# Performance work log

Hardware: AMD Instinct MI355X
Metric: run time of the kernel (lower is better)

Reference implementation:

```python
import jax, jax.numpy as jnp
import numpy as np

N = 100_000      # nodes
E = 1_600_000    # directed input edges (no self loops, unique canonical pairs)
F_IN = 256       # num_features
HID = 128        # 2 * num_hidden (GATConv out width)
NHID = 64        # num_hidden
C = 4            # num_classes
G = 128          # number of graphs in the batch
NEG_SLOPE = 0.2  # PyG GATConv default LeakyReLU slope


def setup_inputs() -> dict:
    key = jax.random.key(0)
    ks = jax.random.split(key, 16)

    # --- graph structure (numpy; deduped canonical pairs so that
    # concat(e, reversed(e)) exactly matches PyG to_undirected+coalesce) ---
    rng = np.random.RandomState(0)
    n_cand = int(E * 1.05)
    s = rng.randint(0, N, size=n_cand)
    off = rng.randint(1, N, size=n_cand)
    d = (s + off) % N                      # guarantees no self loops
    lo, hi = np.minimum(s, d), np.maximum(s, d)
    pairs = np.unique(lo.astype(np.int64) * N + hi.astype(np.int64))[:E]
    src = (pairs // N).astype(np.int64)
    dst = (pairs % N).astype(np.int64)
    edge_index = jnp.asarray(np.stack([src, dst]))  # [2, E]

    batch = jnp.sort(jax.random.randint(ks[0], (N,), 0, G)).astype(jnp.int64)
    x = jax.random.normal(ks[1], (N, F_IN), dtype=jnp.float32)

    sc = 0.05
    params = dict(
        W1=jax.random.normal(ks[2], (HID, F_IN)) * sc,
        as1=jax.random.normal(ks[3], (HID,)) * sc,
        ad1=jax.random.normal(ks[4], (HID,)) * sc,
        b1=jnp.zeros((HID,), jnp.float32),
        W2=jax.random.normal(ks[5], (HID, HID)) * sc,
        as2=jax.random.normal(ks[6], (HID,)) * sc,
        ad2=jax.random.normal(ks[7], (HID,)) * sc,
        b2=jnp.zeros((HID,), jnp.float32),
        fw1=jax.random.normal(ks[8], (NHID, HID)) * sc,
        fb1=jnp.zeros((NHID,), jnp.float32),
        fw2=jax.random.normal(ks[9], (C, NHID)) * sc,
        fb2=jnp.zeros((C,), jnp.float32),
    )
    return dict(x=x, edge_index=edge_index, batch=batch, **params)


def _gat_conv(h_in, src, dst, W, a_src, a_dst, bias):
    """PyG GATConv, heads=1, concat=True. src/dst include self loops."""
    h = h_in @ W.T                                        # [N, out]
    # per-edge attention logits: a_src . h_j + a_dst . h_i
    e = jax.nn.leaky_relu((h @ a_src)[src] + (h @ a_dst)[dst], NEG_SLOPE)
    # edge softmax over incoming edges of each dst node
    m = jax.ops.segment_max(e, dst, num_segments=N)       # [N]
    w = jnp.exp(e - m[dst])
    denom = jax.ops.segment_sum(w, dst, num_segments=N)   # [N] (>0: self loops)
    alpha = w / denom[dst]                                # [Etot]
    out = jax.ops.segment_sum(h[src] * alpha[:, None], dst, num_segments=N)
    return out + bias


def reference(x, edge_index, batch,
              W1, as1, ad1, b1, W2, as2, ad2, b2,
              fw1, fb1, fw2, fb2):
    # to_undirected: input has unique canonical (lo<hi) pairs -> concat exact
    s0, d0 = edge_index[0], edge_index[1]
    loop = jnp.arange(N, dtype=s0.dtype)
    src = jnp.concatenate([s0, d0, loop])  # GATConv adds self loops
    dst = jnp.concatenate([d0, s0, loop])

    h = jax.nn.selu(_gat_conv(x, src, dst, W1, as1, ad1, b1))
    h = jax.nn.selu(_gat_conv(h, src, dst, W2, as2, ad2, b2))

    # global mean pool over graphs
    sums = jax.ops.segment_sum(h, batch, num_segments=G)            # [G, HID]
    cnt = jax.ops.segment_sum(jnp.ones((N,), h.dtype), batch, num_segments=G)
    g = jax.nn.selu(sums / jnp.maximum(cnt, 1.0)[:, None])

    g = jax.nn.selu(g @ fw1.T + fb1)
    # dropout p=0.5 is identity in eval mode
    logits = g @ fw2.T + fb2
    return jax.nn.log_softmax(logits, axis=-1)                      # [G, C]
```

## Files before the change

### kernel.cpp

```cpp
#include <hip/hip_runtime.h>
#include <hip/hip_bf16.h>


#define NN 100000
#define EE 1600000
#define GG 128
#define HID 128
#define AGG_CAP 512
#define NEG_SLOPE 0.2f

typedef short bf16x8 __attribute__((ext_vector_type(8)));
typedef float f32x4 __attribute__((ext_vector_type(4)));

__device__ __forceinline__ float lrelu(float x) { return x > 0.f ? x : NEG_SLOPE * x; }

__device__ __forceinline__ float selu(float x) {
    const float sc = 1.0507009873554805f, al = 1.6732632423543772f;
    return x > 0.f ? sc * x : sc * al * (__expf(x) - 1.f);
}

__device__ __forceinline__ unsigned short f2bf(float x) {
    unsigned int b = __float_as_uint(x);
    b += 0x7FFFu + ((b >> 16) & 1u);
    return (unsigned short)(b >> 16);
}


__global__ __launch_bounds__(256) void castbf_kernel(const float* __restrict__ in,
                                                     unsigned short* __restrict__ out, int n) {
    int i = (blockIdx.x * blockDim.x + threadIdx.x) * 4;
    if (i >= n) return;
    float4 v = *reinterpret_cast<const float4*>(in + i);
    union { unsigned short u[4]; uint2 w; } pk;
    pk.u[0] = f2bf(v.x); pk.u[1] = f2bf(v.y); pk.u[2] = f2bf(v.z); pk.u[3] = f2bf(v.w);
    *reinterpret_cast<uint2*>(out + i) = pk.w;
}


__global__ __launch_bounds__(256) void loptr_kernel(const int* __restrict__ ei,
                                                    int* __restrict__ loptr, int n, int E_) {
    int v = blockIdx.x * blockDim.x + threadIdx.x;
    if (v > n) return;
    int lo = 0, hi = E_;
    while (lo < hi) {
        int mid = (lo + hi) >> 1;
        if (ei[mid] < v) lo = mid + 1; else hi = mid;
    }
    loptr[v] = lo;
}


__global__ void count_kernel(const int* __restrict__ ei, int* __restrict__ deg, int E_) {
    int e = blockIdx.x * blockDim.x + threadIdx.x;
    if (e >= E_) return;
    atomicAdd(&deg[ei[E_ + e]], 1);
}

#define SCAN_CHUNK 512

__global__ __launch_bounds__(256) void block_sum_kernel(const int* __restrict__ deg,
                                                        int* __restrict__ bsum, int n) {
    __shared__ int sd[256];
    int b = blockIdx.x, t = threadIdx.x;
    int base = b * SCAN_CHUNK;
    int v = 0;
    int i0 = base + t, i1 = base + t + 256;
    if (i0 < n) v += deg[i0];
    if (i1 < n) v += deg[i1];
    sd[t] = v;
    __syncthreads();
    for (int off = 128; off; off >>= 1) {
        if (t < off) sd[t] += sd[t + off];
        __syncthreads();
    }
    if (t == 0) bsum[b] = sd[0];
}

__global__ __launch_bounds__(256) void top_scan_kernel(const int* __restrict__ bsum,
                                                       int* __restrict__ boff, int nb,
                                                       int* __restrict__ total_out) {
    __shared__ int a[256], b[256];
    int t = threadIdx.x;
    int v = (t < nb) ? bsum[t] : 0;
    int* cur = a; int* nxt = b;
    cur[t] = v;
    __syncthreads();
    for (int off = 1; off < 256; off <<= 1) {
        int val = cur[t] + ((t >= off) ? cur[t - off] : 0);
        nxt[t] = val;
        __syncthreads();
        int* tmp = cur; cur = nxt; nxt = tmp;
    }
    if (t < nb) boff[t] = cur[t] - v;
    if (t == nb - 1) *total_out = cur[t];
}

__global__ __launch_bounds__(512) void scan_final_kernel(const int* __restrict__ deg,
                                                         const int* __restrict__ boff,
                                                         int* __restrict__ row_ptr,
                                                         int* __restrict__ cursor, int n) {
    __shared__ int a[512], b[512];
    int blk = blockIdx.x, t = threadIdx.x;
    int i = blk * 512 + t;
    int v = (i < n) ? deg[i] : 0;
    int orig = v;
    int* cur = a; int* nxt = b;
    cur[t] = v;
    __syncthreads();
    for (int off = 1; off < 512; off <<= 1) {
        int val = cur[t] + ((t >= off) ? cur[t - off] : 0);
        nxt[t] = val;
        __syncthreads();
        int* tmp = cur; cur = nxt; nxt = tmp;
    }
    if (i < n) {
        int excl = cur[t] - orig + boff[blk];
        row_ptr[i] = excl;
        cursor[i] = excl;
    }
}

__global__ void scatter_kernel(const int* __restrict__ ei, int* __restrict__ cursor,
                               int* __restrict__ csr, int E_) {
    int e = blockIdx.x * blockDim.x + threadIdx.x;
    if (e >= E_) return;
    int u = ei[e], v = ei[E_ + e];
    int p = atomicAdd(&cursor[v], 1);
    csr[p] = u;
}


template<int K, bool BF16IN>
__global__ __launch_bounds__(256) void mfma_gemm(const void* __restrict__ Ain,
                                                 const unsigned short* __restrict__ Wb,
                                                 float* __restrict__ C,
                                                 unsigned short* __restrict__ Cb,
                                                 int M) {
    __shared__ unsigned short As[128 * 32];
    __shared__ unsigned short Bs[128 * 32];
    int tid = threadIdx.x;
    int brow = blockIdx.x * 128;
    int w = tid >> 6, lane = tid & 63;
    int wr = (w >> 1) * 64, wc = (w & 1) * 64;
    int l15 = lane & 15, g = lane >> 4;

    const f32x4 zero = {0.f, 0.f, 0.f, 0.f};
    f32x4 acc[4][4];
    #pragma unroll
    for (int m = 0; m < 4; ++m)
        #pragma unroll
        for (int n = 0; n < 4; ++n) acc[m][n] = zero;

    int srow = tid >> 2;
    int slot = tid & 3;

    for (int k0 = 0; k0 < K; k0 += 32) {
        #pragma unroll
        for (int half = 0; half < 2; ++half) {
            int r = srow + half * 64;
            int grow = brow + r;
            union { unsigned short u[8]; uint4 v; } pk;
            if (BF16IN) {
                const unsigned short* A16 = (const unsigned short*)Ain;
                if (grow < M)
                    pk.v = *reinterpret_cast<const uint4*>(A16 + (size_t)grow * K + k0 + slot * 8);
                else pk.v = make_uint4(0, 0, 0, 0);
            } else {
                const float* A32 = (const float*)Ain;
                if (grow < M) {
                    const float4* p = reinterpret_cast<const float4*>(A32 + (size_t)grow * K + k0 + slot * 8);
                    float4 f0 = p[0], f1 = p[1];
                    pk.u[0] = f2bf(f0.x); pk.u[1] = f2bf(f0.y);
                    pk.u[2] = f2bf(f0.z); pk.u[3] = f2bf(f0.w);
                    pk.u[4] = f2bf(f1.x); pk.u[5] = f2bf(f1.y);
                    pk.u[6] = f2bf(f1.z); pk.u[7] = f2bf(f1.w);
                } else pk.v = make_uint4(0, 0, 0, 0);
            }
            int ss = slot ^ (r & 3);
            *reinterpret_cast<uint4*>(&As[r * 32 + ss * 8]) = pk.v;
        }
        #pragma unroll
        for (int half = 0; half < 2; ++half) {
            int r = srow + half * 64;
            uint4 v = *reinterpret_cast<const uint4*>(Wb + (size_t)r * K + k0 + slot * 8);
            int ss = slot ^ (r & 3);
            *reinterpret_cast<uint4*>(&Bs[r * 32 + ss * 8]) = v;
        }
        __syncthreads();

        bf16x8 af[4], bfr[4];
        #pragma unroll
        for (int m = 0; m < 4; ++m) {
            int row = wr + m * 16 + l15;
            af[m] = *reinterpret_cast<const bf16x8*>(&As[row * 32 + ((g ^ (row & 3)) * 8)]);
        }
        #pragma unroll
        for (int n = 0; n < 4; ++n) {
            int col = wc + n * 16 + l15;
            bfr[n] = *reinterpret_cast<const bf16x8*>(&Bs[col * 32 + ((g ^ (col & 3)) * 8)]);
        }
        #pragma unroll
        for (int m = 0; m < 4; ++m)
            #pragma unroll
            for (int n = 0; n < 4; ++n)
                acc[m][n] = __builtin_amdgcn_mfma_f32_16x16x32_bf16(af[m], bfr[n], acc[m][n], 0, 0, 0);
        __syncthreads();
    }

    #pragma unroll
    for (int m = 0; m < 4; ++m) {
        int rbase = brow + wr + m * 16 + g * 4;
        #pragma unroll
        for (int j = 0; j < 4; ++j) {
            int row = rbase + j;
            if (row < M) {
                #pragma unroll
                for (int n = 0; n < 4; ++n) {
                    int col = wc + n * 16 + l15;
                    float val = acc[m][n][j];
                    C[(size_t)row * 128 + col] = val;
                    Cb[(size_t)row * 128 + col] = f2bf(val);
                }
            }
        }
    }
}


__global__ __launch_bounds__(256) void hshd_kernel(const float* __restrict__ h,
                                                   const float* __restrict__ a_src,
                                                   const float* __restrict__ a_dst,
                                                   float* __restrict__ hs, float* __restrict__ hd,
                                                   int n) {
    int w = (blockIdx.x * blockDim.x + threadIdx.x) >> 6;
    int lane = threadIdx.x & 63;
    if (w >= n) return;
    float2 hv = reinterpret_cast<const float2*>(h + (size_t)w * 128)[lane];
    float2 as2 = reinterpret_cast<const float2*>(a_src)[lane];
    float2 ad2 = reinterpret_cast<const float2*>(a_dst)[lane];
    float ps = hv.x * as2.x + hv.y * as2.y;
    float pd = hv.x * ad2.x + hv.y * ad2.y;
    #pragma unroll
    for (int off = 32; off; off >>= 1) {
        ps += __shfl_xor(ps, off);
        pd += __shfl_xor(pd, off);
    }
    if (lane == 0) { hs[w] = ps; hd[w] = pd; }
}


__global__ __launch_bounds__(256) void agg_kernel(const float* __restrict__ h,
                                                  const unsigned int* __restrict__ hb32,
                                                  const float* __restrict__ hs,
                                                  const float* __restrict__ hd,
                                                  const int* __restrict__ loptr,
                                                  const int* __restrict__ eiD,
                                                  const int* __restrict__ hiptr,
                                                  const int* __restrict__ csr,
                                                  const float* __restrict__ bias,
                                                  float* __restrict__ out,
                                                  unsigned int* __restrict__ outb,
                                                  int n) {
    __shared__ float esh[4][AGG_CAP];
    __shared__ int ush[4][AGG_CAP];
    int wib = threadIdx.x >> 6;
    int lane = threadIdx.x & 63;
    int v = blockIdx.x * 4 + wib;
    if (v >= n) return;
    int s_lo = loptr[v];
    int dlo = loptr[v + 1] - s_lo;
    int s_hi = hiptr[v];
    int d = dlo + (hiptr[v + 1] - s_hi);
    float hdv = hd[v];
    float e_self = lrelu(hs[v] + hdv);
    float m, inv;
    bool fits = (d <= AGG_CAP);

    auto nbr = [&](int k) -> int {
        return (k < dlo) ? eiD[s_lo + k] : csr[s_hi + k - dlo];
    };
    auto gx = [&](int u) -> float2 {
        unsigned int w = hb32[(size_t)u * 64 + lane];
        return make_float2(__uint_as_float(w << 16), __uint_as_float(w & 0xFFFF0000u));
    };

    if (fits) {
        float mloc = -3.4e38f;
        for (int k = lane; k < d; k += 64) {
            int u = nbr(k);
            float e = lrelu(hs[u] + hdv);
            ush[wib][k] = u;
            esh[wib][k] = e;
            mloc = fmaxf(mloc, e);
        }
        #pragma unroll
        for (int off = 32; off; off >>= 1) mloc = fmaxf(mloc, __shfl_xor(mloc, off));
        m = fmaxf(mloc, e_self);
        float sloc = 0.f;
        for (int k = lane; k < d; k += 64) sloc += __expf(esh[wib][k] - m);
        #pragma unroll
        for (int off = 32; off; off >>= 1) sloc += __shfl_xor(sloc, off);
        float s = sloc + __expf(e_self - m);
        inv = 1.f / s;
        for (int k = lane; k < d; k += 64) esh[wib][k] = __expf(esh[wib][k] - m) * inv;
    } else {
        float mloc = -3.4e38f;
        for (int k = lane; k < d; k += 64) mloc = fmaxf(mloc, lrelu(hs[nbr(k)] + hdv));
        #pragma unroll
        for (int off = 32; off; off >>= 1) mloc = fmaxf(mloc, __shfl_xor(mloc, off));
        m = fmaxf(mloc, e_self);
        float sloc = 0.f;
        for (int k = lane; k < d; k += 64) sloc += __expf(lrelu(hs[nbr(k)] + hdv) - m);
        #pragma unroll
        for (int off = 32; off; off >>= 1) sloc += __shfl_xor(sloc, off);
        float s = sloc + __expf(e_self - m);
        inv = 1.f / s;
    }
    __syncthreads();

    float2 hvv = reinterpret_cast<const float2*>(h + (size_t)v * 128)[lane];
    float a_self = __expf(e_self - m) * inv;
    float accx = a_self * hvv.x;
    float accy = a_self * hvv.y;
    if (fits) {
        int k = 0;
        for (; k + 4 <= d; k += 4) {
            float a0 = esh[wib][k + 0], a1 = esh[wib][k + 1];
            float a2 = esh[wib][k + 2], a3 = esh[wib][k + 3];
            int u0 = ush[wib][k + 0], u1 = ush[wib][k + 1];
            int u2 = ush[wib][k + 2], u3 = ush[wib][k + 3];
            float2 x0 = gx(u0);
            float2 x1 = gx(u1);
            float2 x2 = gx(u2);
            float2 x3 = gx(u3);
            accx = fmaf(a0, x0.x, accx); accy = fmaf(a0, x0.y, accy);
            accx = fmaf(a1, x1.x, accx); accy = fmaf(a1, x1.y, accy);
            accx = fmaf(a2, x2.x, accx); accy = fmaf(a2, x2.y, accy);
            accx = fmaf(a3, x3.x, accx); accy = fmaf(a3, x3.y, accy);
        }
        for (; k < d; ++k) {
            float al = esh[wib][k];
            float2 xv = gx(ush[wib][k]);
            accx = fmaf(al, xv.x, accx);
            accy = fmaf(al, xv.y, accy);
        }
    } else {
        for (int k = 0; k < d; ++k) {
            int u = nbr(k);
            float al = __expf(lrelu(hs[u] + hdv) - m) * inv;
            float2 xv = gx(u);
            accx = fmaf(al, xv.x, accx);
            accy = fmaf(al, xv.y, accy);
        }
    }
    float2 bb = reinterpret_cast<const float2*>(bias)[lane];
    float o0 = selu(accx + bb.x);
    float o1 = selu(accy + bb.y);
    reinterpret_cast<float2*>(out + (size_t)v * 128)[lane] = make_float2(o0, o1);
    unsigned int pb = ((unsigned int)f2bf(o1) << 16) | (unsigned int)f2bf(o0);
    outb[(size_t)v * 64 + lane] = pb;
}


__device__ __forceinline__ int lower_bound_dev(const int* __restrict__ b, int n, int val) {
    int lo = 0, hi = n;
    while (lo < hi) {
        int mid = (lo + hi) >> 1;
        if (b[mid] < val) lo = mid + 1; else hi = mid;
    }
    return lo;
}

__global__ __launch_bounds__(1024) void pool_mlp_kernel(const float* __restrict__ h,
                                                        const int* __restrict__ batch,
                                                        const float* __restrict__ fw1,
                                                        const float* __restrict__ fb1,
                                                        const float* __restrict__ fw2,
                                                        const float* __restrict__ fb2,
                                                        float* __restrict__ out, int n) {
    int g = blockIdx.x;
    int t = threadIdx.x;
    int lane = t & 63;
    int rg = t >> 6;
    __shared__ float2 sm[16][64];
    __shared__ float gv[128];
    __shared__ float hid[64];
    __shared__ float logits[4];

    int s = lower_bound_dev(batch, n, g);
    int e = lower_bound_dev(batch, n, g + 1);

    float2 acc = make_float2(0.f, 0.f);
    const float2* h2 = reinterpret_cast<const float2*>(h);
    int i = s + rg;
    for (; i + 16 < e; i += 32) {
        float2 v0 = h2[(size_t)i * 64 + lane];
        float2 v1 = h2[(size_t)(i + 16) * 64 + lane];
        acc.x += v0.x + v1.x;
        acc.y += v0.y + v1.y;
    }
    for (; i < e; i += 16) {
        float2 v0 = h2[(size_t)i * 64 + lane];
        acc.x += v0.x;
        acc.y += v0.y;
    }
    sm[rg][lane] = acc;
    __syncthreads();
    if (rg == 0) {
        float2 tot = make_float2(0.f, 0.f);
        #pragma unroll
        for (int r = 0; r < 16; ++r) {
            tot.x += sm[r][lane].x;
            tot.y += sm[r][lane].y;
        }
        float cnt = fmaxf((float)(e - s), 1.0f);
        gv[lane * 2 + 0] = selu(tot.x / cnt);
        gv[lane * 2 + 1] = selu(tot.y / cnt);
    }
    __syncthreads();
    if (t < 64) {
        float a = fb1[t];
        for (int k = 0; k < 128; ++k) a = fmaf(fw1[t * 128 + k], gv[k], a);
        hid[t] = selu(a);
    }
    __syncthreads();
    if (t < 4) {
        float a = fb2[t];
        for (int k = 0; k < 64; ++k) a = fmaf(fw2[t * 64 + k], hid[k], a);
        logits[t] = a;
    }
    __syncthreads();
    if (t < 4) {
        float mx = fmaxf(fmaxf(logits[0], logits[1]), fmaxf(logits[2], logits[3]));
        float sum = __expf(logits[0] - mx) + __expf(logits[1] - mx) +
                    __expf(logits[2] - mx) + __expf(logits[3] - mx);
        out[g * 4 + t] = logits[t] - mx - logf(sum);
    }
}


extern "C" void kernel_launch(void* const* d_in, const int* in_sizes, int n_in,
                              void* d_out, int out_size, void* d_ws, size_t ws_size,
                              hipStream_t stream) {
    const float* x   = (const float*)d_in[0];
    const int*   ei  = (const int*)d_in[1];
    const int*   bat = (const int*)d_in[2];
    const float* W1  = (const float*)d_in[3];
    const float* as1 = (const float*)d_in[4];
    const float* ad1 = (const float*)d_in[5];
    const float* b1  = (const float*)d_in[6];
    const float* W2  = (const float*)d_in[7];
    const float* as2 = (const float*)d_in[8];
    const float* ad2 = (const float*)d_in[9];
    const float* b2  = (const float*)d_in[10];
    const float* fw1 = (const float*)d_in[11];
    const float* fb1 = (const float*)d_in[12];
    const float* fw2 = (const float*)d_in[13];
    const float* fb2 = (const float*)d_in[14];
    float* out = (float*)d_out;

    char* ws = (char*)d_ws;
    size_t off = 0;
    auto alloc = [&](size_t bytes) {
        void* p = ws + off;
        off += (bytes + 255) & ~(size_t)255;
        return p;
    };
    float*          bufA    = (float*)alloc((size_t)NN * 128 * 4);
    float*          bufB    = (float*)alloc((size_t)NN * 128 * 4);
    unsigned short* hb      = (unsigned short*)alloc((size_t)NN * 128 * 2);
    unsigned short* hbB     = (unsigned short*)alloc((size_t)NN * 128 * 2);
    unsigned short* wb1     = (unsigned short*)alloc((size_t)HID * 256 * 2);
    unsigned short* wb2     = (unsigned short*)alloc((size_t)HID * 128 * 2);
    float*          hs      = (float*)alloc((size_t)NN * 4);
    float*          hd      = (float*)alloc((size_t)NN * 4);
    int*            deg     = (int*)alloc((size_t)NN * 4);
    int*            row_ptr = (int*)alloc((size_t)(NN + 1) * 4);
    int*            cursor  = (int*)alloc((size_t)NN * 4);
    int*            loptr   = (int*)alloc((size_t)(NN + 1) * 4);
    int*            csr     = (int*)alloc((size_t)EE * 4);
    int*            bsum    = (int*)alloc(256 * 4);
    int*            boff    = (int*)alloc(256 * 4);

    hipMemsetAsync(deg, 0, (size_t)NN * 4, stream);
    loptr_kernel<<<(NN + 1 + 255) / 256, 256, 0, stream>>>(ei, loptr, NN, EE);
    count_kernel<<<(EE + 255) / 256, 256, 0, stream>>>(ei, deg, EE);
    int NB = (NN + SCAN_CHUNK - 1) / SCAN_CHUNK;
    block_sum_kernel<<<NB, 256, 0, stream>>>(deg, bsum, NN);
    top_scan_kernel<<<1, 256, 0, stream>>>(bsum, boff, NB, row_ptr + NN);
    scan_final_kernel<<<NB, 512, 0, stream>>>(deg, boff, row_ptr, cursor, NN);
    scatter_kernel<<<(EE + 255) / 256, 256, 0, stream>>>(ei, cursor, csr, EE);

    castbf_kernel<<<(HID * 256 / 4 + 255) / 256, 256, 0, stream>>>(W1, wb1, HID * 256);
    castbf_kernel<<<(HID * 128 / 4 + 255) / 256, 256, 0, stream>>>(W2, wb2, HID * 128);

    const int* eiD = ei + EE;
    int gemmGrid = (NN + 127) / 128;

    mfma_gemm<256, false><<<gemmGrid, 256, 0, stream>>>(x, wb1, bufA, hb, NN);
    hshd_kernel<<<((size_t)NN * 64 + 255) / 256, 256, 0, stream>>>(bufA, as1, ad1, hs, hd, NN);
    agg_kernel<<<(NN + 3) / 4, 256, 0, stream>>>(bufA, (const unsigned int*)hb, hs, hd,
                                                 loptr, eiD, row_ptr, csr, b1, bufB,
                                                 (unsigned int*)hbB, NN);

    mfma_gemm<128, true><<<gemmGrid, 256, 0, stream>>>(hbB, wb2, bufA, hb, NN);
    hshd_kernel<<<((size_t)NN * 64 + 255) / 256, 256, 0, stream>>>(bufA, as2, ad2, hs, hd, NN);
    agg_kernel<<<(NN + 3) / 4, 256, 0, stream>>>(bufA, (const unsigned int*)hb, hs, hd,
                                                 loptr, eiD, row_ptr, csr, b2, bufB,
                                                 (unsigned int*)hbB, NN);

    pool_mlp_kernel<<<GG, 1024, 0, stream>>>(bufB, bat, fw1, fb1, fw2, fb2, out, NN);
}
```

Before: 739.8 us.

## Two-pass bucketed CSR scatter and deepen aggregation gather unroll

The single random scatter that builds the CSR is replaced by two passes. Edges are first binned into 128-node destination buckets via per-bucket atomic cursors into a temporary (u,v) array, then a second pass does the per-node atomic placement. Because bucketed edges are locally clustered, the second pass's atomics and csr writes should hit nearby addresses. The aggregation inner loop is also unrolled from 4 to 8 neighbors to put more gathers in flight, at the cost of an extra 12.8MB temp buffer, two extra launches and higher register pressure.

```diff
diff --git a/kernel.cpp b/kernel.cpp
--- a/kernel.cpp
+++ b/kernel.cpp
@@ -8,6 +8,8 @@
 #define HID 128
 #define AGG_CAP 512
 #define NEG_SLOPE 0.2f
+#define BKT_SHIFT 7
+#define NBKT ((NN + 127) >> 7)
 
 typedef short bf16x8 __attribute__((ext_vector_type(8)));
 typedef float f32x4 __attribute__((ext_vector_type(4)));
@@ -120,13 +122,32 @@
     }
 }
 
-__global__ void scatter_kernel(const int* __restrict__ ei, int* __restrict__ cursor,
-                               int* __restrict__ csr, int E_) {
+
+__global__ __launch_bounds__(256) void bcur_init_kernel(const int* __restrict__ row_ptr,
+                                                        int* __restrict__ bcur) {
+    int b = blockIdx.x * blockDim.x + threadIdx.x;
+    if (b < NBKT) bcur[b] = row_ptr[b << BKT_SHIFT];
+}
+
+__global__ __launch_bounds__(256) void binA_kernel(const int* __restrict__ ei,
+                                                   int* __restrict__ bcur,
+                                                   uint2* __restrict__ tmp, int E_) {
     int e = blockIdx.x * blockDim.x + threadIdx.x;
     if (e >= E_) return;
     int u = ei[e], v = ei[E_ + e];
-    int p = atomicAdd(&cursor[v], 1);
-    csr[p] = u;
+    int b = v >> BKT_SHIFT;
+    int p = atomicAdd(&bcur[b], 1);
+    tmp[p] = make_uint2((unsigned)u, (unsigned)v);
+}
+
+__global__ __launch_bounds__(256) void binB_kernel(const uint2* __restrict__ tmp,
+                                                   int* __restrict__ cursor,
+                                                   int* __restrict__ csr, int E_) {
+    int i = blockIdx.x * blockDim.x + threadIdx.x;
+    if (i >= E_) return;
+    uint2 t = tmp[i];
+    int p = atomicAdd(&cursor[t.y], 1);
+    csr[p] = (int)t.x;
 }
 
 
@@ -324,19 +345,17 @@
     float accy = a_self * hvv.y;
     if (fits) {
         int k = 0;
-        for (; k + 4 <= d; k += 4) {
-            float a0 = esh[wib][k + 0], a1 = esh[wib][k + 1];
-            float a2 = esh[wib][k + 2], a3 = esh[wib][k + 3];
-            int u0 = ush[wib][k + 0], u1 = ush[wib][k + 1];
-            int u2 = ush[wib][k + 2], u3 = ush[wib][k + 3];
-            float2 x0 = gx(u0);
-            float2 x1 = gx(u1);
-            float2 x2 = gx(u2);
-            float2 x3 = gx(u3);
-            accx = fmaf(a0, x0.x, accx); accy = fmaf(a0, x0.y, accy);
-            accx = fmaf(a1, x1.x, accx); accy = fmaf(a1, x1.y, accy);
-            accx = fmaf(a2, x2.x, accx); accy = fmaf(a2, x2.y, accy);
-            accx = fmaf(a3, x3.x, accx); accy = fmaf(a3, x3.y, accy);
+        for (; k + 8 <= d; k += 8) {
+            float a_[8]; int u_[8]; float2 x_[8];
+            #pragma unroll
+            for (int j = 0; j < 8; ++j) { a_[j] = esh[wib][k + j]; u_[j] = ush[wib][k + j]; }
+            #pragma unroll
+            for (int j = 0; j < 8; ++j) x_[j] = gx(u_[j]);
+            #pragma unroll
+            for (int j = 0; j < 8; ++j) {
+                accx = fmaf(a_[j], x_[j].x, accx);
+                accy = fmaf(a_[j], x_[j].y, accy);
+            }
         }
         for (; k < d; ++k) {
             float al = esh[wib][k];
@@ -479,6 +498,8 @@
     int*            cursor  = (int*)alloc((size_t)NN * 4);
     int*            loptr   = (int*)alloc((size_t)(NN + 1) * 4);
     int*            csr     = (int*)alloc((size_t)EE * 4);
+    uint2*          tmp     = (uint2*)alloc((size_t)EE * 8);
+    int*            bcur    = (int*)alloc((size_t)NBKT * 4);
     int*            bsum    = (int*)alloc(256 * 4);
     int*            boff    = (int*)alloc(256 * 4);
 
@@ -489,7 +510,9 @@
     block_sum_kernel<<<NB, 256, 0, stream>>>(deg, bsum, NN);
     top_scan_kernel<<<1, 256, 0, stream>>>(bsum, boff, NB, row_ptr + NN);
     scan_final_kernel<<<NB, 512, 0, stream>>>(deg, boff, row_ptr, cursor, NN);
-    scatter_kernel<<<(EE + 255) / 256, 256, 0, stream>>>(ei, cursor, csr, EE);
+    bcur_init_kernel<<<(NBKT + 255) / 256, 256, 0, stream>>>(row_ptr, bcur);
+    binA_kernel<<<(EE + 255) / 256, 256, 0, stream>>>(ei, bcur, tmp, EE);
+    binB_kernel<<<(EE + 255) / 256, 256, 0, stream>>>(tmp, cursor, csr, EE);
 
     castbf_kernel<<<(HID * 256 / 4 + 255) / 256, 256, 0, stream>>>(W1, wb1, HID * 256);
     castbf_kernel<<<(HID * 128 / 4 + 255) / 256, 256, 0, stream>>>(W2, wb2, HID * 128);
```

Measured after the change: 1.150 ms. 55.5% more time.

## Fuse attention-logit dots into GEMM epilogue and drop fp32 activation buffers

Applied to the files above, without the earlier changes.

The per-node attention projections (h·a_src, h·a_dst) are now computed in the MFMA GEMM epilogue from the accumulators, using shuffle and shared-memory reductions, which removes the separate hshd kernel. All fp32 copies of the activations are removed: the aggregation reads its self term from bf16 and writes only bf16 output, and pooling reads bf16. The aggregation gather loop is also unrolled to 8 neighbors to keep more loads in flight. This cuts global memory traffic substantially, at the cost of slightly lower precision for the self term and the pooled sums.

```diff
diff --git a/kernel.cpp b/kernel.cpp
--- a/kernel.cpp
+++ b/kernel.cpp
@@ -133,15 +133,21 @@
 template<int K, bool BF16IN>
 __global__ __launch_bounds__(256) void mfma_gemm(const void* __restrict__ Ain,
                                                  const unsigned short* __restrict__ Wb,
-                                                 float* __restrict__ C,
+                                                 const float* __restrict__ avs,
+                                                 const float* __restrict__ avd,
                                                  unsigned short* __restrict__ Cb,
+                                                 float* __restrict__ hs,
+                                                 float* __restrict__ hd,
                                                  int M) {
     __shared__ unsigned short As[128 * 32];
     __shared__ unsigned short Bs[128 * 32];
+    __shared__ float hsp[128][2];
+    __shared__ float hdp[128][2];
     int tid = threadIdx.x;
     int brow = blockIdx.x * 128;
     int w = tid >> 6, lane = tid & 63;
     int wr = (w >> 1) * 64, wc = (w & 1) * 64;
+    int whalf = w & 1;
     int l15 = lane & 15, g = lane >> 4;
 
     const f32x4 zero = {0.f, 0.f, 0.f, 0.f};
@@ -217,40 +223,53 @@
                 #pragma unroll
                 for (int n = 0; n < 4; ++n) {
                     int col = wc + n * 16 + l15;
-                    float val = acc[m][n][j];
-                    C[(size_t)row * 128 + col] = val;
-                    Cb[(size_t)row * 128 + col] = f2bf(val);
+                    Cb[(size_t)row * 128 + col] = f2bf(acc[m][n][j]);
                 }
             }
         }
     }
-}
-
-
-__global__ __launch_bounds__(256) void hshd_kernel(const float* __restrict__ h,
-                                                   const float* __restrict__ a_src,
-                                                   const float* __restrict__ a_dst,
-                                                   float* __restrict__ hs, float* __restrict__ hd,
-                                                   int n) {
-    int w = (blockIdx.x * blockDim.x + threadIdx.x) >> 6;
-    int lane = threadIdx.x & 63;
-    if (w >= n) return;
-    float2 hv = reinterpret_cast<const float2*>(h + (size_t)w * 128)[lane];
-    float2 as2 = reinterpret_cast<const float2*>(a_src)[lane];
-    float2 ad2 = reinterpret_cast<const float2*>(a_dst)[lane];
-    float ps = hv.x * as2.x + hv.y * as2.y;
-    float pd = hv.x * ad2.x + hv.y * ad2.y;
+
+    float asv[4], adv[4];
     #pragma unroll
-    for (int off = 32; off; off >>= 1) {
-        ps += __shfl_xor(ps, off);
-        pd += __shfl_xor(pd, off);
-    }
-    if (lane == 0) { hs[w] = ps; hd[w] = pd; }
-}
-
-
-__global__ __launch_bounds__(256) void agg_kernel(const float* __restrict__ h,
-                                                  const unsigned int* __restrict__ hb32,
+    for (int n = 0; n < 4; ++n) {
+        asv[n] = avs[wc + n * 16 + l15];
+        adv[n] = avd[wc + n * 16 + l15];
+    }
+    #pragma unroll
+    for (int m = 0; m < 4; ++m) {
+        #pragma unroll
+        for (int j = 0; j < 4; ++j) {
+            float vs = 0.f, vd = 0.f;
+            #pragma unroll
+            for (int n = 0; n < 4; ++n) {
+                float a = acc[m][n][j];
+                vs = fmaf(a, asv[n], vs);
+                vd = fmaf(a, adv[n], vd);
+            }
+            #pragma unroll
+            for (int off = 1; off < 16; off <<= 1) {
+                vs += __shfl_xor(vs, off);
+                vd += __shfl_xor(vd, off);
+            }
+            if (l15 == 0) {
+                int rl = wr + m * 16 + g * 4 + j;
+                hsp[rl][whalf] = vs;
+                hdp[rl][whalf] = vd;
+            }
+        }
+    }
+    __syncthreads();
+    if (tid < 128) {
+        int row = brow + tid;
+        if (row < M) {
+            hs[row] = hsp[tid][0] + hsp[tid][1];
+            hd[row] = hdp[tid][0] + hdp[tid][1];
+        }
+    }
+}
+
+
+__global__ __launch_bounds__(256) void agg_kernel(const unsigned int* __restrict__ hb32,
                                                   const float* __restrict__ hs,
                                                   const float* __restrict__ hd,
                                                   const int* __restrict__ loptr,
@@ -258,7 +277,6 @@
                                                   const int* __restrict__ hiptr,
                                                   const int* __restrict__ csr,
                                                   const float* __restrict__ bias,
-                                                  float* __restrict__ out,
                                                   unsigned int* __restrict__ outb,
                                                   int n) {
     __shared__ float esh[4][AGG_CAP];
@@ -318,25 +336,23 @@
     }
     __syncthreads();
 
-    float2 hvv = reinterpret_cast<const float2*>(h + (size_t)v * 128)[lane];
+    float2 hvv = gx(v);
     float a_self = __expf(e_self - m) * inv;
     float accx = a_self * hvv.x;
     float accy = a_self * hvv.y;
     if (fits) {
         int k = 0;
-        for (; k + 4 <= d; k += 4) {
-            float a0 = esh[wib][k + 0], a1 = esh[wib][k + 1];
-            float a2 = esh[wib][k + 2], a3 = esh[wib][k + 3];
-            int u0 = ush[wib][k + 0], u1 = ush[wib][k + 1];
-            int u2 = ush[wib][k + 2], u3 = ush[wib][k + 3];
-            float2 x0 = gx(u0);
-            float2 x1 = gx(u1);
-            float2 x2 = gx(u2);
-            float2 x3 = gx(u3);
-            accx = fmaf(a0, x0.x, accx); accy = fmaf(a0, x0.y, accy);
-            accx = fmaf(a1, x1.x, accx); accy = fmaf(a1, x1.y, accy);
-            accx = fmaf(a2, x2.x, accx); accy = fmaf(a2, x2.y, accy);
-            accx = fmaf(a3, x3.x, accx); accy = fmaf(a3, x3.y, accy);
+        for (; k + 8 <= d; k += 8) {
+            float a_[8]; int u_[8]; float2 x_[8];
+            #pragma unroll
+            for (int j = 0; j < 8; ++j) { a_[j] = esh[wib][k + j]; u_[j] = ush[wib][k + j]; }
+            #pragma unroll
+            for (int j = 0; j < 8; ++j) x_[j] = gx(u_[j]);
+            #pragma unroll
+            for (int j = 0; j < 8; ++j) {
+                accx = fmaf(a_[j], x_[j].x, accx);
+                accy = fmaf(a_[j], x_[j].y, accy);
+            }
         }
         for (; k < d; ++k) {
             float al = esh[wib][k];
@@ -356,7 +372,6 @@
     float2 bb = reinterpret_cast<const float2*>(bias)[lane];
     float o0 = selu(accx + bb.x);
     float o1 = selu(accy + bb.y);
-    reinterpret_cast<float2*>(out + (size_t)v * 128)[lane] = make_float2(o0, o1);
     unsigned int pb = ((unsigned int)f2bf(o1) << 16) | (unsigned int)f2bf(o0);
     outb[(size_t)v * 64 + lane] = pb;
 }
@@ -371,7 +386,7 @@
     return lo;
 }
 
-__global__ __launch_bounds__(1024) void pool_mlp_kernel(const float* __restrict__ h,
+__global__ __launch_bounds__(1024) void pool_mlp_kernel(const unsigned int* __restrict__ hb,
                                                         const int* __restrict__ batch,
                                                         const float* __restrict__ fw1,
                                                         const float* __restrict__ fb1,
@@ -391,18 +406,17 @@
     int e = lower_bound_dev(batch, n, g + 1);
 
     float2 acc = make_float2(0.f, 0.f);
-    const float2* h2 = reinterpret_cast<const float2*>(h);
     int i = s + rg;
     for (; i + 16 < e; i += 32) {
-        float2 v0 = h2[(size_t)i * 64 + lane];
-        float2 v1 = h2[(size_t)(i + 16) * 64 + lane];
-        acc.x += v0.x + v1.x;
-        acc.y += v0.y + v1.y;
+        unsigned int w0 = hb[(size_t)i * 64 + lane];
+        unsigned int w1 = hb[(size_t)(i + 16) * 64 + lane];
+        acc.x += __uint_as_float(w0 << 16) + __uint_as_float(w1 << 16);
+        acc.y += __uint_as_float(w0 & 0xFFFF0000u) + __uint_as_float(w1 & 0xFFFF0000u);
     }
     for (; i < e; i += 16) {
-        float2 v0 = h2[(size_t)i * 64 + lane];
-        acc.x += v0.x;
-        acc.y += v0.y;
+        unsigned int w0 = hb[(size_t)i * 64 + lane];
+        acc.x += __uint_as_float(w0 << 16);
+        acc.y += __uint_as_float(w0 & 0xFFFF0000u);
     }
     sm[rg][lane] = acc;
     __syncthreads();
@@ -466,8 +480,6 @@
         off += (bytes + 255) & ~(size_t)255;
         return p;
     };
-    float*          bufA    = (float*)alloc((size_t)NN * 128 * 4);
-    float*          bufB    = (float*)alloc((size_t)NN * 128 * 4);
     unsigned short* hb      = (unsigned short*)alloc((size_t)NN * 128 * 2);
     unsigned short* hbB     = (unsigned short*)alloc((size_t)NN * 128 * 2);
     unsigned short* wb1     = (unsigned short*)alloc((size_t)HID * 256 * 2);
@@ -497,17 +509,16 @@
     const int* eiD = ei + EE;
     int gemmGrid = (NN + 127) / 128;
 
-    mfma_gemm<256, false><<<gemmGrid, 256, 0, stream>>>(x, wb1, bufA, hb, NN);
-    hshd_kernel<<<((size_t)NN * 64 + 255) / 256, 256, 0, stream>>>(bufA, as1, ad1, hs, hd, NN);
-    agg_kernel<<<(NN + 3) / 4, 256, 0, stream>>>(bufA, (const unsigned int*)hb, hs, hd,
-                                                 loptr, eiD, row_ptr, csr, b1, bufB,
+    mfma_gemm<256, false><<<gemmGrid, 256, 0, stream>>>(x, wb1, as1, ad1, hb, hs, hd, NN);
+    agg_kernel<<<(NN + 3) / 4, 256, 0, stream>>>((const unsigned int*)hb, hs, hd,
+                                                 loptr, eiD, row_ptr, csr, b1,
                                                  (unsigned int*)hbB, NN);
 
-    mfma_gemm<128, true><<<gemmGrid, 256, 0, stream>>>(hbB, wb2, bufA, hb, NN);
-    hshd_kernel<<<((size_t)NN * 64 + 255) / 256, 256, 0, stream>>>(bufA, as2, ad2, hs, hd, NN);
-    agg_kernel<<<(NN + 3) / 4, 256, 0, stream>>>(bufA, (const unsigned int*)hb, hs, hd,
-                                                 loptr, eiD, row_ptr, csr, b2, bufB,
+    mfma_gemm<128, true><<<gemmGrid, 256, 0, stream>>>(hbB, wb2, as2, ad2, hb, hs, hd, NN);
+    agg_kernel<<<(NN + 3) / 4, 256, 0, stream>>>((const unsigned int*)hb, hs, hd,
+                                                 loptr, eiD, row_ptr, csr, b2,
                                                  (unsigned int*)hbB, NN);
 
-    pool_mlp_kernel<<<GG, 1024, 0, stream>>>(bufB, bat, fw1, fb1, fw2, fb2, out, NN);
-}
+    pool_mlp_kernel<<<GG, 1024, 0, stream>>>((const unsigned int*)hbB, bat,
+                                             fw1, fb1, fw2, fb2, out, NN);
+}
```

New measurement: 682.9 us. 1.08x faster.
